# Kernel tuning notes

Measured on AMD Instinct MI355X. Metric: run time of the kernel, lower is better.

The kernel has to match this reference:

```python
import jax, jax.numpy as jnp
import numpy as np

N_NODES = 50000
N_EDGES = 800000
DIM_IN = 64
DIM_HID = 128
DIM_OUT = 64


def _linear_init(key, fan_in, fan_out):
    # torch nn.Linear default: U(-1/sqrt(fan_in), 1/sqrt(fan_in)) for W and b
    kw, kb = jax.random.split(key)
    bound = 1.0 / np.sqrt(fan_in)
    W = jax.random.uniform(kw, (fan_in, fan_out), minval=-bound, maxval=bound, dtype=jnp.float32)
    b = jax.random.uniform(kb, (fan_out,), minval=-bound, maxval=bound, dtype=jnp.float32)
    return W, b


def setup_inputs() -> dict:
    key = jax.random.key(0)
    kx, ke, k0, k1, k2 = jax.random.split(key, 5)
    x = jax.random.normal(kx, (N_NODES, DIM_IN), dtype=jnp.float32)
    edge_idx = jax.random.randint(ke, (2, N_EDGES), 0, N_NODES, dtype=jnp.int64)
    W0, b0 = _linear_init(k0, 2 * DIM_IN, DIM_HID)
    W1, b1 = _linear_init(k1, DIM_HID, DIM_HID)
    W2, b2 = _linear_init(k2, DIM_HID, DIM_OUT)
    return {"x": x, "edge_idx": edge_idx, "W0": W0, "b0": b0,
            "W1": W1, "b1": b1, "W2": W2, "b2": b2}


def reference(x, edge_idx, W0, b0, W1, b1, W2, b2):
    row, col = edge_idx[0], edge_idx[1]
    # gather + concat edge features: [E, 2*dim_in]
    h = jnp.concatenate([x[row], x[col]], axis=-1)
    h = jax.nn.softplus(h @ W0 + b0)
    h = jax.nn.softplus(h @ W1 + b1)
    h = h @ W2 + b2  # [E, dim_out]
    # scatter-add edge messages to source nodes
    return jax.ops.segment_sum(h, row, num_segments=x.shape[0])
```

## Files before the change

### kernel.cpp

```cpp
#include <hip/hip_runtime.h>
#include <math.h>

#define N_NODES 50000
#define N_EDGES 800000
#define DIM_IN 64
#define DIM_HID 128
#define DIM_OUT 64

#define EB  128
#define PAD 136

typedef __attribute__((ext_vector_type(8))) short short8;
typedef __attribute__((ext_vector_type(4))) float f32x4;

__device__ __forceinline__ unsigned short f2bf(float f) {
    unsigned u = __float_as_uint(f);
    return (unsigned short)((u + 0x7fffu + ((u >> 16) & 1u)) >> 16);
}

__device__ __forceinline__ short8 pack8(float4 a, float4 b) {
    short8 f;
    f[0] = (short)f2bf(a.x); f[1] = (short)f2bf(a.y);
    f[2] = (short)f2bf(a.z); f[3] = (short)f2bf(a.w);
    f[4] = (short)f2bf(b.x); f[5] = (short)f2bf(b.y);
    f[6] = (short)f2bf(b.z); f[7] = (short)f2bf(b.w);
    return f;
}

__device__ __forceinline__ float softplus_f(float v) {
    float e = __expf(-fabsf(v));
    return fmaxf(v, 0.0f) + __logf(1.0f + e);
}

__global__ void prep_weights(const float* __restrict__ W0,
                             const float* __restrict__ W1,
                             const float* __restrict__ W2,
                             unsigned short* __restrict__ wt) {
    const int R = 128 * PAD;
    int i = blockIdx.x * blockDim.x + threadIdx.x;
    if (i < R) {
        int n = i / PAD, k = i - n * PAD;
        wt[i] = f2bf(k < 128 ? W0[k * DIM_HID + n] : 0.f);
    } else if (i < 2 * R) {
        int j = i - R;
        int n = j / PAD, k = j - n * PAD;
        wt[i] = f2bf(k < 128 ? W1[k * DIM_HID + n] : 0.f);
    } else if (i < 2 * R + 64 * PAD) {
        int j = i - 2 * R;
        int n = j / PAD, k = j - n * PAD;
        wt[i] = f2bf(k < 128 ? W2[k * DIM_OUT + n] : 0.f);
    }
}

template <int NT>
__device__ __forceinline__ void mfma_layer(const short8 afr[2][4],
                                           const unsigned short* __restrict__ W,
                                           const float* __restrict__ bias,
                                           f32x4 acc[2][8], int l16, int q) {
#pragma unroll
    for (int t = 0; t < NT; ++t) {
        float bv = bias[t * 16 + l16];
#pragma unroll
        for (int m = 0; m < 2; ++m)
            acc[m][t] = (f32x4){bv, bv, bv, bv};
    }
#pragma unroll
    for (int t = 0; t < NT; ++t) {
        const unsigned short* Wp = W + (t * 16 + l16) * PAD + q * 8;
        short8 bfr[4];
#pragma unroll
        for (int kk = 0; kk < 4; ++kk)
            bfr[kk] = *(const short8*)(Wp + kk * 32);
#pragma unroll
        for (int m = 0; m < 2; ++m)
#pragma unroll
            for (int kk = 0; kk < 4; ++kk)
                acc[m][t] = __builtin_amdgcn_mfma_f32_16x16x32_bf16(
                    afr[m][kk], bfr[kk], acc[m][t], 0, 0, 0);
    }
}

__global__ __launch_bounds__(256, 3)
void edge_mlp_mfma(const float* __restrict__ x,
                   const int* __restrict__ eidx,
                   const unsigned short* __restrict__ wt,
                   const float* __restrict__ b0,
                   const float* __restrict__ b1,
                   const float* __restrict__ b2,
                   float* __restrict__ out) {
    __shared__ unsigned short Ha[4][32 * PAD];

    const int tid  = threadIdx.x;
    const int lane = tid & 63;
    const int w    = tid >> 6;
    const int l16  = lane & 15;
    const int q    = lane >> 4;
    const int e0w  = blockIdx.x * EB + w * 32;
    unsigned short* Hw = &Ha[w][0];

    const unsigned short* Wt0 = wt;
    const unsigned short* Wt1 = wt + 128 * PAD;
    const unsigned short* Wt2 = wt + 256 * PAD;

    int rowI[2], colI[2];
#pragma unroll
    for (int m = 0; m < 2; ++m) {
        rowI[m] = eidx[e0w + m * 16 + l16];
        colI[m] = eidx[N_EDGES + e0w + m * 16 + l16];
    }

    short8 afr[2][4];
#pragma unroll
    for (int m = 0; m < 2; ++m)
#pragma unroll
        for (int kk = 0; kk < 4; ++kk) {
            int node = (kk < 2) ? rowI[m] : colI[m];
            const float* p = x + (size_t)node * DIM_IN + (kk & 1) * 32 + q * 8;
            float4 va = *(const float4*)p;
            float4 vb = *(const float4*)(p + 4);
            afr[m][kk] = pack8(va, vb);
        }

    f32x4 acc[2][8];
    mfma_layer<8>(afr, Wt0, b0, acc, l16, q);

#pragma unroll
    for (int m = 0; m < 2; ++m)
#pragma unroll
        for (int t = 0; t < 8; ++t)
#pragma unroll
            for (int r = 0; r < 4; ++r)
                Hw[(m * 16 + q * 4 + r) * PAD + t * 16 + l16] =
                    f2bf(softplus_f(acc[m][t][r]));
    asm volatile("s_waitcnt lgkmcnt(0)" ::: "memory");

#pragma unroll
    for (int m = 0; m < 2; ++m)
#pragma unroll
        for (int kk = 0; kk < 4; ++kk)
            afr[m][kk] = *(const short8*)(Hw + (m * 16 + l16) * PAD + kk * 32 + q * 8);

    mfma_layer<8>(afr, Wt1, b1, acc, l16, q);

#pragma unroll
    for (int m = 0; m < 2; ++m)
#pragma unroll
        for (int t = 0; t < 8; ++t)
#pragma unroll
            for (int r = 0; r < 4; ++r)
                Hw[(m * 16 + q * 4 + r) * PAD + t * 16 + l16] =
                    f2bf(softplus_f(acc[m][t][r]));
    asm volatile("s_waitcnt lgkmcnt(0)" ::: "memory");

#pragma unroll
    for (int m = 0; m < 2; ++m)
#pragma unroll
        for (int kk = 0; kk < 4; ++kk)
            afr[m][kk] = *(const short8*)(Hw + (m * 16 + l16) * PAD + kk * 32 + q * 8);

    mfma_layer<4>(afr, Wt2, b2, acc, l16, q);

#pragma unroll
    for (int m = 0; m < 2; ++m)
#pragma unroll
        for (int r = 0; r < 4; ++r) {
            int node = eidx[e0w + m * 16 + q * 4 + r];
            float* op = out + (size_t)node * DIM_OUT + l16;
            atomicAdd(op,      acc[m][0][r]);
            atomicAdd(op + 16, acc[m][1][r]);
            atomicAdd(op + 32, acc[m][2][r]);
            atomicAdd(op + 48, acc[m][3][r]);
        }
}

extern "C" void kernel_launch(void* const* d_in, const int* in_sizes, int n_in,
                              void* d_out, int out_size, void* d_ws, size_t ws_size,
                              hipStream_t stream) {
    const float* x  = (const float*)d_in[0];
    const int*   ei = (const int*)d_in[1];
    const float* W0 = (const float*)d_in[2];
    const float* b0 = (const float*)d_in[3];
    const float* W1 = (const float*)d_in[4];
    const float* b1 = (const float*)d_in[5];
    const float* W2 = (const float*)d_in[6];
    const float* b2 = (const float*)d_in[7];
    float* out = (float*)d_out;
    unsigned short* wt = (unsigned short*)d_ws;

    hipMemsetAsync(out, 0, (size_t)N_NODES * DIM_OUT * sizeof(float), stream);

    const int wn = 2 * 128 * PAD + 64 * PAD;
    prep_weights<<<(wn + 255) / 256, 256, 0, stream>>>(W0, W1, W2, wt);

    edge_mlp_mfma<<<N_EDGES / EB, 256, 0, stream>>>(x, ei, wt, b0, b1, b2, out);
}
```

Baseline: 306.8 us.

## Keep hidden activations in registers via transposed MFMA and permuted weight rows

Swaps the MFMA operand order so each layer's output fragment already matches the next layer's input fragment layout. The weight K dimension is permuted at prep time to make that work, which removes the LDS round trip for hidden activations. Softplus now uses exp2 with a polynomial in place of log1p, bf16 conversion uses packed cvt, and occupancy is raised to 4 waves per SIMD. Atomics now write 4 contiguous floats per lane. The polynomial softplus is less accurate, and dropping LDS traffic may increase register pressure.

```diff
diff --git a/kernel.cpp b/kernel.cpp
--- a/kernel.cpp
+++ b/kernel.cpp
@@ -6,81 +6,63 @@
 #define DIM_IN 64
 #define DIM_HID 128
 #define DIM_OUT 64
-
-#define EB  128
 #define PAD 136
 
 typedef __attribute__((ext_vector_type(8))) short short8;
 typedef __attribute__((ext_vector_type(4))) float f32x4;
+
+union U8 { uint4 u; short8 s; };
 
 __device__ __forceinline__ unsigned short f2bf(float f) {
     unsigned u = __float_as_uint(f);
     return (unsigned short)((u + 0x7fffu + ((u >> 16) & 1u)) >> 16);
 }
 
-__device__ __forceinline__ short8 pack8(float4 a, float4 b) {
-    short8 f;
-    f[0] = (short)f2bf(a.x); f[1] = (short)f2bf(a.y);
-    f[2] = (short)f2bf(a.z); f[3] = (short)f2bf(a.w);
-    f[4] = (short)f2bf(b.x); f[5] = (short)f2bf(b.y);
-    f[6] = (short)f2bf(b.z); f[7] = (short)f2bf(b.w);
-    return f;
+__device__ __forceinline__ unsigned cvt_pk_bf16(float a, float b) {
+#if __has_builtin(__builtin_amdgcn_cvt_pk_bf16_f32)
+    auto pk = __builtin_amdgcn_cvt_pk_bf16_f32(a, b);
+    unsigned d; __builtin_memcpy(&d, &pk, 4);
+    return d;
+#else
+    return (unsigned)f2bf(a) | ((unsigned)f2bf(b) << 16);
+#endif
 }
 
-__device__ __forceinline__ float softplus_f(float v) {
-    float e = __expf(-fabsf(v));
-    return fmaxf(v, 0.0f) + __logf(1.0f + e);
+__device__ __forceinline__ float exp2_fast(float a) {
+#if __has_builtin(__builtin_amdgcn_exp2f)
+    return __builtin_amdgcn_exp2f(a);
+#else
+    return __expf(a * 0.69314718f);
+#endif
+}
+
+__device__ __forceinline__ unsigned sp2(float x0, float x1) {
+    const float L2E = 1.44269504f;
+    float z0 = exp2_fast(-fabsf(x0) * L2E);
+    float z1 = exp2_fast(-fabsf(x1) * L2E);
+    float p0 = fmaf(fmaf(fmaf(-0.1011458f, z0, 0.2942925f), z0, -0.5f), z0, 1.0f) * z0;
+    float p1 = fmaf(fmaf(fmaf(-0.1011458f, z1, 0.2942925f), z1, -0.5f), z1, 1.0f) * z1;
+    return cvt_pk_bf16(fmaxf(x0, 0.0f) + p0, fmaxf(x1, 0.0f) + p1);
 }
 
 __global__ void prep_weights(const float* __restrict__ W0,
                              const float* __restrict__ W1,
                              const float* __restrict__ W2,
                              unsigned short* __restrict__ wt) {
-    const int R = 128 * PAD;
     int i = blockIdx.x * blockDim.x + threadIdx.x;
-    if (i < R) {
-        int n = i / PAD, k = i - n * PAD;
-        wt[i] = f2bf(k < 128 ? W0[k * DIM_HID + n] : 0.f);
-    } else if (i < 2 * R) {
-        int j = i - R;
-        int n = j / PAD, k = j - n * PAD;
-        wt[i] = f2bf(k < 128 ? W1[k * DIM_HID + n] : 0.f);
-    } else if (i < 2 * R + 64 * PAD) {
-        int j = i - 2 * R;
-        int n = j / PAD, k = j - n * PAD;
-        wt[i] = f2bf(k < 128 ? W2[k * DIM_OUT + n] : 0.f);
+    if (i >= 320 * PAD) return;
+    int row = i / PAD, s = i - row * PAD;
+    float v = 0.f;
+    if (s < 128) {
+        int f = ((s >> 5) << 5) | (((s & 7) >> 2) << 4) | (((s >> 3) & 3) << 2) | (s & 3);
+        if (row < 128)      v = W0[s * DIM_HID + row];
+        else if (row < 256) v = W1[f * DIM_HID + (row - 128)];
+        else                v = W2[f * DIM_OUT + (row - 256)];
     }
+    wt[i] = f2bf(v);
 }
 
-template <int NT>
-__device__ __forceinline__ void mfma_layer(const short8 afr[2][4],
-                                           const unsigned short* __restrict__ W,
-                                           const float* __restrict__ bias,
-                                           f32x4 acc[2][8], int l16, int q) {
-#pragma unroll
-    for (int t = 0; t < NT; ++t) {
-        float bv = bias[t * 16 + l16];
-#pragma unroll
-        for (int m = 0; m < 2; ++m)
-            acc[m][t] = (f32x4){bv, bv, bv, bv};
-    }
-#pragma unroll
-    for (int t = 0; t < NT; ++t) {
-        const unsigned short* Wp = W + (t * 16 + l16) * PAD + q * 8;
-        short8 bfr[4];
-#pragma unroll
-        for (int kk = 0; kk < 4; ++kk)
-            bfr[kk] = *(const short8*)(Wp + kk * 32);
-#pragma unroll
-        for (int m = 0; m < 2; ++m)
-#pragma unroll
-            for (int kk = 0; kk < 4; ++kk)
-                acc[m][t] = __builtin_amdgcn_mfma_f32_16x16x32_bf16(
-                    afr[m][kk], bfr[kk], acc[m][t], 0, 0, 0);
-    }
-}
-
-__global__ __launch_bounds__(256, 3)
+__global__ __launch_bounds__(256, 4)
 void edge_mlp_mfma(const float* __restrict__ x,
                    const int* __restrict__ eidx,
                    const unsigned short* __restrict__ wt,
@@ -88,89 +70,99 @@
                    const float* __restrict__ b1,
                    const float* __restrict__ b2,
                    float* __restrict__ out) {
-    __shared__ unsigned short Ha[4][32 * PAD];
-
-    const int tid  = threadIdx.x;
-    const int lane = tid & 63;
-    const int w    = tid >> 6;
+    const int lane = threadIdx.x & 63;
+    const int w    = threadIdx.x >> 6;
     const int l16  = lane & 15;
     const int q    = lane >> 4;
-    const int e0w  = blockIdx.x * EB + w * 32;
-    unsigned short* Hw = &Ha[w][0];
+    const int e0w  = blockIdx.x * 128 + w * 32;
 
     const unsigned short* Wt0 = wt;
     const unsigned short* Wt1 = wt + 128 * PAD;
     const unsigned short* Wt2 = wt + 256 * PAD;
 
-    int rowI[2], colI[2];
+    int nodeR[2], nodeC[2];
 #pragma unroll
     for (int m = 0; m < 2; ++m) {
-        rowI[m] = eidx[e0w + m * 16 + l16];
-        colI[m] = eidx[N_EDGES + e0w + m * 16 + l16];
+        nodeR[m] = eidx[e0w + m * 16 + l16];
+        nodeC[m] = eidx[N_EDGES + e0w + m * 16 + l16];
     }
 
-    short8 afr[2][4];
+    short8 hfr[2][4];
 #pragma unroll
     for (int m = 0; m < 2; ++m)
 #pragma unroll
         for (int kk = 0; kk < 4; ++kk) {
-            int node = (kk < 2) ? rowI[m] : colI[m];
+            int node = (kk >= 2) ? nodeC[m] : nodeR[m];
             const float* p = x + (size_t)node * DIM_IN + (kk & 1) * 32 + q * 8;
-            float4 va = *(const float4*)p;
-            float4 vb = *(const float4*)(p + 4);
-            afr[m][kk] = pack8(va, vb);
+            float4 v0 = *(const float4*)p;
+            float4 v1 = *(const float4*)(p + 4);
+            U8 t;
+            t.u.x = cvt_pk_bf16(v0.x, v0.y);
+            t.u.y = cvt_pk_bf16(v0.z, v0.w);
+            t.u.z = cvt_pk_bf16(v1.x, v1.y);
+            t.u.w = cvt_pk_bf16(v1.z, v1.w);
+            hfr[m][kk] = t.s;
         }
 
-    f32x4 acc[2][8];
-    mfma_layer<8>(afr, Wt0, b0, acc, l16, q);
+#pragma unroll
+    for (int L = 0; L < 2; ++L) {
+        const unsigned short* W = L ? Wt1 : Wt0;
+        const float* bias = L ? b1 : b0;
+        unsigned d[2][8][2];
+#pragma unroll
+        for (int ti = 0; ti < 8; ++ti) {
+            f32x4 bb = *(const f32x4*)(bias + ti * 16 + q * 4);
+            f32x4 a0 = bb, a1 = bb;
+            const unsigned short* Wp = W + (ti * 16 + l16) * PAD + q * 8;
+            short8 wf[4];
+#pragma unroll
+            for (int kk = 0; kk < 4; ++kk)
+                wf[kk] = *(const short8*)(Wp + kk * 32);
+#pragma unroll
+            for (int kk = 0; kk < 4; ++kk) {
+                a0 = __builtin_amdgcn_mfma_f32_16x16x32_bf16(wf[kk], hfr[0][kk], a0, 0, 0, 0);
+                a1 = __builtin_amdgcn_mfma_f32_16x16x32_bf16(wf[kk], hfr[1][kk], a1, 0, 0, 0);
+            }
+            d[0][ti][0] = sp2(a0[0], a0[1]);
+            d[0][ti][1] = sp2(a0[2], a0[3]);
+            d[1][ti][0] = sp2(a1[0], a1[1]);
+            d[1][ti][1] = sp2(a1[2], a1[3]);
+        }
+#pragma unroll
+        for (int m = 0; m < 2; ++m)
+#pragma unroll
+            for (int kk = 0; kk < 4; ++kk) {
+                U8 t;
+                t.u.x = d[m][2 * kk][0];
+                t.u.y = d[m][2 * kk][1];
+                t.u.z = d[m][2 * kk + 1][0];
+                t.u.w = d[m][2 * kk + 1][1];
+                hfr[m][kk] = t.s;
+            }
+    }
 
 #pragma unroll
-    for (int m = 0; m < 2; ++m)
-#pragma unroll
-        for (int t = 0; t < 8; ++t)
-#pragma unroll
-            for (int r = 0; r < 4; ++r)
-                Hw[(m * 16 + q * 4 + r) * PAD + t * 16 + l16] =
-                    f2bf(softplus_f(acc[m][t][r]));
-    asm volatile("s_waitcnt lgkmcnt(0)" ::: "memory");
-
-#pragma unroll
-    for (int m = 0; m < 2; ++m)
+    for (int ti = 0; ti < 4; ++ti) {
+        f32x4 bb = *(const f32x4*)(b2 + ti * 16 + q * 4);
+        f32x4 a0 = bb, a1 = bb;
+        const unsigned short* Wp = Wt2 + (ti * 16 + l16) * PAD + q * 8;
+        short8 wf[4];
 #pragma unroll
         for (int kk = 0; kk < 4; ++kk)
-            afr[m][kk] = *(const short8*)(Hw + (m * 16 + l16) * PAD + kk * 32 + q * 8);
-
-    mfma_layer<8>(afr, Wt1, b1, acc, l16, q);
-
+            wf[kk] = *(const short8*)(Wp + kk * 32);
 #pragma unroll
-    for (int m = 0; m < 2; ++m)
-#pragma unroll
-        for (int t = 0; t < 8; ++t)
-#pragma unroll
-            for (int r = 0; r < 4; ++r)
-                Hw[(m * 16 + q * 4 + r) * PAD + t * 16 + l16] =
-                    f2bf(softplus_f(acc[m][t][r]));
-    asm volatile("s_waitcnt lgkmcnt(0)" ::: "memory");
-
-#pragma unroll
-    for (int m = 0; m < 2; ++m)
-#pragma unroll
-        for (int kk = 0; kk < 4; ++kk)
-            afr[m][kk] = *(const short8*)(Hw + (m * 16 + l16) * PAD + kk * 32 + q * 8);
-
-    mfma_layer<4>(afr, Wt2, b2, acc, l16, q);
-
-#pragma unroll
-    for (int m = 0; m < 2; ++m)
+        for (int kk = 0; kk < 4; ++kk) {
+            a0 = __builtin_amdgcn_mfma_f32_16x16x32_bf16(wf[kk], hfr[0][kk], a0, 0, 0, 0);
+            a1 = __builtin_amdgcn_mfma_f32_16x16x32_bf16(wf[kk], hfr[1][kk], a1, 0, 0, 0);
+        }
+        float* p0 = out + (size_t)nodeR[0] * DIM_OUT + ti * 16 + q * 4;
+        float* p1 = out + (size_t)nodeR[1] * DIM_OUT + ti * 16 + q * 4;
 #pragma unroll
         for (int r = 0; r < 4; ++r) {
-            int node = eidx[e0w + m * 16 + q * 4 + r];
-            float* op = out + (size_t)node * DIM_OUT + l16;
-            atomicAdd(op,      acc[m][0][r]);
-            atomicAdd(op + 16, acc[m][1][r]);
-            atomicAdd(op + 32, acc[m][2][r]);
-            atomicAdd(op + 48, acc[m][3][r]);
+            atomicAdd(p0 + r, a0[r]);
+            atomicAdd(p1 + r, a1[r]);
         }
+    }
 }
 
 extern "C" void kernel_launch(void* const* d_in, const int* in_sizes, int n_in,
@@ -189,8 +181,8 @@
 
     hipMemsetAsync(out, 0, (size_t)N_NODES * DIM_OUT * sizeof(float), stream);
 
-    const int wn = 2 * 128 * PAD + 64 * PAD;
+    const int wn = 320 * PAD;
     prep_weights<<<(wn + 255) / 256, 256, 0, stream>>>(W0, W1, W2, wt);
 
-    edge_mlp_mfma<<<N_EDGES / EB, 256, 0, stream>>>(x, ei, wt, b0, b1, b2, out);
+    edge_mlp_mfma<<<N_EDGES / 128, 256, 0, stream>>>(x, ei, wt, b0, b1, b2, out);
 }
```

Result: slower. 772.7 us (+151.8%).
